# Kernel tuning notes

Measured on AMD Instinct MI355X. Metric: run time of the kernel, lower is better.

The kernel has to match this reference:

```python
import jax, jax.numpy as jnp
import numpy as np

B, C, H, W = 4, 128, 56, 56
K = 7
K2 = K * K
RATIO = 16


def _conv1x1(x, w, b=None):
    # x: [B,C,H,W], w: [O,C]
    y = jnp.einsum('oc,bchw->bohw', w, x)
    return y if b is None else y + b[None, :, None, None]


def _dwconv(x, w, dil, pad):
    # depthwise conv, w: [C,1,k,k]
    return jax.lax.conv_general_dilated(
        x, w, window_strides=(1, 1), padding=[(pad, pad), (pad, pad)],
        rhs_dilation=(dil, dil), feature_group_count=x.shape[1],
        dimension_numbers=('NCHW', 'OIHW', 'NCHW'))


def _bn(x, s, b):
    # inference-mode BatchNorm folded to per-channel affine
    return x * s[None, :, None, None] + b[None, :, None, None]


def setup_inputs() -> dict:
    key = jax.random.key(0)
    ks = jax.random.split(key, 16)
    w = 0.05  # weight scale
    inp = {
        'x_up': jax.random.normal(ks[0], (B, C, H, W), jnp.float32),
        'x_skip': jax.random.normal(ks[1], (B, C, H, W), jnp.float32),
        'wq': jax.random.normal(ks[2], (C, C), jnp.float32) * w,
        'bq': jnp.zeros((C,), jnp.float32),
        'wk': jax.random.normal(ks[3], (C, C), jnp.float32) * w,
        'bk': jnp.zeros((C,), jnp.float32),
        'wv': jax.random.normal(ks[4], (C, C), jnp.float32) * w,
        'bv': jnp.zeros((C,), jnp.float32),
        'ww': jax.random.normal(ks[5], (K2, 49), jnp.float32) * w,
        'bw': jnp.zeros((K2,), jnp.float32),
        'lk_w': jax.random.normal(ks[6], (C, 1, K, K), jnp.float32) * 0.1,
        'lk_bn_s': jax.random.uniform(ks[7], (C,), jnp.float32, 0.5, 1.5),
        'lk_bn_b': jnp.zeros((C,), jnp.float32),
        'dw5': jax.random.normal(ks[8], (C, 1, 5, 5), jnp.float32) * 0.1,
        'bn5_s': jax.random.uniform(ks[7], (C,), jnp.float32, 0.5, 1.5),
        'bn5_b': jnp.zeros((C,), jnp.float32),
        'dw3a': jax.random.normal(ks[9], (C, 1, 3, 3), jnp.float32) * 0.1,
        'bn3a_s': jax.random.uniform(ks[9], (C,), jnp.float32, 0.5, 1.5),
        'bn3a_b': jnp.zeros((C,), jnp.float32),
        'dw3b': jax.random.normal(ks[10], (C, 1, 3, 3), jnp.float32) * 0.1,
        'bn3b_s': jax.random.uniform(ks[10], (C,), jnp.float32, 0.5, 1.5),
        'bn3b_b': jnp.zeros((C,), jnp.float32),
        'dw3c': jax.random.normal(ks[11], (C, 1, 3, 3), jnp.float32) * 0.1,
        'bn3c_s': jax.random.uniform(ks[11], (C,), jnp.float32, 0.5, 1.5),
        'bn3c_b': jnp.zeros((C,), jnp.float32),
        'lepe_bn_s': jax.random.uniform(ks[12], (C,), jnp.float32, 0.5, 1.5),
        'lepe_bn_b': jnp.zeros((C,), jnp.float32),
        'gate_w': jax.random.normal(ks[13], (C, C), jnp.float32) * w,
        'gate_bn_s': jax.random.uniform(ks[13], (C,), jnp.float32, 0.5, 1.5),
        'gate_bn_b': jnp.zeros((C,), jnp.float32),
        'fus_w': jax.random.normal(ks[14], (C, C), jnp.float32) * w,
        'fus_b': jnp.zeros((C,), jnp.float32),
        'ca_w1': jax.random.normal(ks[15], (C // RATIO, C), jnp.float32) * w,
        'ca_w2': jax.random.normal(ks[15], (C, C // RATIO), jnp.float32) * w,
        'res_scale': jnp.ones((1,), jnp.float32),
    }
    return inp


def _forward(x_up, x_skip, wq, bq, wk, bk, wv, bv, ww, bw,
             lk_w, lk_bn_s, lk_bn_b, dw5, bn5_s, bn5_b,
             dw3a, bn3a_s, bn3a_b, dw3b, bn3b_s, bn3b_b, dw3c, bn3c_s, bn3c_b,
             lepe_bn_s, lepe_bn_b, gate_w, gate_bn_s, gate_bn_b,
             fus_w, fus_b, ca_w1, ca_w2, res_scale):
    identity = x_skip

    # ---- lepe: DilatedReparamBlock (lk 7x7 dw + 4 dilated dw branches, each BN) + final BN
    out = _bn(_dwconv(x_skip, lk_w, 1, 3), lk_bn_s, lk_bn_b)
    out = out + _bn(_dwconv(x_skip, dw5, 1, 2), bn5_s, bn5_b)    # k=5, d=1
    out = out + _bn(_dwconv(x_skip, dw3a, 1, 1), bn3a_s, bn3a_b)  # k=3, d=1
    out = out + _bn(_dwconv(x_skip, dw3b, 2, 2), bn3b_s, bn3b_b)  # k=3, d=2
    out = out + _bn(_dwconv(x_skip, dw3c, 3, 3), bn3c_s, bn3c_b)  # k=3, d=3
    lepe = _bn(out, lepe_bn_s, lepe_bn_b)

    # ---- gate: 1x1 conv (no bias) -> BN -> SiLU
    gate = jax.nn.silu(_bn(_conv1x1(x_skip, gate_w), gate_bn_s, gate_bn_b))

    # ---- q / k / v
    query = _conv1x1(x_skip, wq, bq)                              # [B,C,H,W]
    # AdaptiveAvgPool2d(7): H,W divisible by 7 -> block mean
    pooled = x_up.reshape(B, C, 7, H // 7, 7, W // 7).mean(axis=(3, 5))  # [B,C,7,7]
    key_t = _conv1x1(pooled, wk, bk).reshape(B, C, 49)            # [B,C,49]
    value = _conv1x1(x_skip, wv, bv)                              # [B,C,H,W]

    # ---- attention over 49 pooled key tokens
    scale = float(C) ** -0.5
    q_r = query.reshape(B, C, H * W).transpose(0, 2, 1)           # [B,HW,C]
    attn = jax.nn.softmax(jnp.einsum('bnc,bcl->bnl', q_r, key_t) * scale, axis=-1)
    attn_r = attn.transpose(0, 2, 1).reshape(B, 49, H, W)         # [B,49,H,W]
    dyn_w = jnp.einsum('ol,blhw->bohw', ww, attn_r) + bw[None, :, None, None]  # [B,K2,H,W]

    # ---- unfold value (k=7, pad=3), torch layout: channel-major, (kh,kw) row-major
    pad = K // 2
    vp = jnp.pad(value, ((0, 0), (0, 0), (pad, pad), (pad, pad)))
    patches = jnp.stack([vp[:, :, i:i + H, j:j + W]
                         for i in range(K) for j in range(K)], axis=2)  # [B,C,K2,H,W]
    mixed = jnp.einsum('bkhw,bckhw->bchw', dyn_w, patches)

    x_fused = _conv1x1(mixed, fus_w, fus_b) + lepe

    # ---- channel attention (shared MLP on avg & max pooled)
    avg = x_fused.mean(axis=(2, 3))                               # [B,C]
    mx = x_fused.max(axis=(2, 3))                                 # [B,C]
    def ca_mlp(v):
        return jnp.einsum('cr,br->bc', ca_w2, jax.nn.relu(jnp.einsum('rc,bc->br', ca_w1, v)))
    ca = jax.nn.sigmoid(ca_mlp(avg) + ca_mlp(mx))[:, :, None, None]
    x_fused = ca * x_fused

    return gate * x_fused + identity * res_scale


def reference(x_up, x_skip, wq, bq, wk, bk, wv, bv, ww, bw,
              lk_w, lk_bn_s, lk_bn_b, dw5, bn5_s, bn5_b,
              dw3a, bn3a_s, bn3a_b, dw3b, bn3b_s, bn3b_b, dw3c, bn3c_s, bn3c_b,
              lepe_bn_s, lepe_bn_b, gate_w, gate_bn_s, gate_bn_b,
              fus_w, fus_b, ca_w1, ca_w2, res_scale):
    return _forward(x_up, x_skip, wq, bq, wk, bk, wv, bv, ww, bw,
                    lk_w, lk_bn_s, lk_bn_b, dw5, bn5_s, bn5_b,
                    dw3a, bn3a_s, bn3a_b, dw3b, bn3b_s, bn3b_b, dw3c, bn3c_s, bn3c_b,
                    lepe_bn_s, lepe_bn_b, gate_w, gate_bn_s, gate_bn_b,
                    fus_w, fus_b, ca_w1, ca_w2, res_scale)
```

## Files before the change

### kernel.cpp

```cpp
#include <hip/hip_runtime.h>

typedef unsigned int u32;

#define HW 3136
#define SCALE 0.08838834764831843f

#define OFF_W7    0
#define OFF_BIAS  6272
#define OFF_POOL  6400
#define OFF_MT    31488
#define OFF_D     56576
#define OFF_AVG   56772
#define OFF_MAXU  57284
#define OFF_CA    57796
#define OFF_WC    58308
#define OFF_BC    74692
#define OFF_WQKT  74820
#define OFF_DQ    91204
#define OFF_VB    91332
#define OFF_S0    91460
#define OFF_FV    91464
#define OFF_DYN   1697096
#define OFF_XF    2311752

struct Params {
  const float *x_up, *x_skip, *wq, *bq, *wk, *bk, *wv, *bv, *ww, *bw;
  const float *lk_w, *lk_s, *lk_b, *dw5, *s5, *b5, *dw3a, *s3a, *b3a,
              *dw3b, *s3b, *b3b, *dw3c, *s3c, *b3c, *lepe_s, *lepe_b;
  const float *gate_w, *gate_s, *gate_b, *fus_w, *fus_b, *ca_w1, *ca_w2, *res;
  float* W;
  float* out;
};

__device__ __forceinline__ u32 fenc(float f){
  union{float f; u32 u;} v; v.f = f;
  return (v.u & 0x80000000u) ? ~v.u : (v.u | 0x80000000u);
}
__device__ __forceinline__ float fdec(u32 u){
  union{float f; u32 uu;} v;
  v.uu = (u & 0x80000000u) ? (u ^ 0x80000000u) : ~u;
  return v.f;
}

__global__ __launch_bounds__(256) void k_prep_w(Params P){
  float* W = P.W;
  const int tid = threadIdx.x, blk = blockIdx.x;
  if (blk < 64){
    const int o = blk*2 + (tid >> 7), c = tid & 127;
    float a = 0.f;
    #pragma unroll 8
    for (int m=0;m<128;++m) a += P.fus_w[o*128+m] * P.wv[m*128+c];
    W[OFF_WC + o*128 + c] = a;
  } else if (blk < 128){
    const int c = (blk-64)*2 + (tid >> 7), k = tid & 127;
    float a = 0.f;
    #pragma unroll 8
    for (int o=0;o<128;++o) a += P.wq[o*128+k] * P.wk[o*128+c];
    W[OFF_WQKT + c*128 + k] = a;
  } else if (blk == 128){
    for (int idx = tid; idx < 6272; idx += 256){
      const int c = idx/49, k = idx%49;
      const int dy = k/7 - 3, dx = k%7 - 3;
      float w = P.lk_s[c] * P.lk_w[c*49 + k];
      if (dy>=-2 && dy<=2 && dx>=-2 && dx<=2)
        w += P.s5[c] * P.dw5[c*25 + (dy+2)*5 + (dx+2)];
      if (dy>=-1 && dy<=1 && dx>=-1 && dx<=1)
        w += P.s3a[c] * P.dw3a[c*9 + (dy+1)*3 + (dx+1)];
      if ((dy==-2||dy==0||dy==2) && (dx==-2||dx==0||dx==2))
        w += P.s3b[c] * P.dw3b[c*9 + (dy/2+1)*3 + (dx/2+1)];
      if ((dy==-3||dy==0||dy==3) && (dx==-3||dx==0||dx==3))
        w += P.s3c[c] * P.dw3c[c*9 + (dy/3+1)*3 + (dx/3+1)];
      W[OFF_W7 + idx] = P.lepe_s[c] * w;
    }
    if (tid < 128){
      const float bs = P.lk_b[tid] + P.b5[tid] + P.b3a[tid] + P.b3b[tid] + P.b3c[tid];
      W[OFF_BIAS + tid] = P.lepe_s[tid] * bs + P.lepe_b[tid] + P.fus_b[tid];
    }
    for (int i = tid; i < 512; i += 256){
      W[OFF_AVG + i] = 0.f;
      ((u32*)W + OFF_MAXU)[i] = fenc(-1e30f);
    }
  } else {
    if (tid < 128){
      float bc = 0.f, dq = 0.f, vb = 0.f;
      #pragma unroll 8
      for (int m=0;m<128;++m){
        bc += P.fus_w[tid*128+m] * P.bv[m];
        dq += P.wq[m*128+tid] * P.bk[m];
        vb += P.bq[m] * P.wk[m*128+tid];
      }
      W[OFF_BC + tid] = bc;
      W[OFF_DQ + tid] = dq;
      W[OFF_VB + tid] = vb;
      if (tid == 0){
        float s = 0.f;
        for (int m=0;m<128;++m) s += P.bq[m]*P.bk[m];
        W[OFF_S0] = s;
      }
    }
  }
}

__global__ __launch_bounds__(256) void k_pool(Params P){
  __shared__ float pl[3136];
  __shared__ float part[208];
  float* W = P.W;
  const int tid = threadIdx.x, blk = blockIdx.x;
  const int b = blk >> 7, c = blk & 127;
  const float* src = P.x_up + (size_t)(b*128 + c)*HW;
  for (int idx = tid; idx < 784; idx += 256)
    *(float4*)&pl[idx*4] = *(const float4*)(src + idx*4);
  __syncthreads();
  if (tid < 196){
    const int l = tid >> 2, s = tid & 3;
    const int i = l/7, j = l%7;
    float sm = 0.f;
    #pragma unroll
    for (int r=0;r<2;++r){
      const int base = (8*i + 2*s + r)*56 + 8*j;
      #pragma unroll
      for (int e=0;e<8;++e) sm += pl[base+e];
    }
    part[tid] = sm;
  }
  __syncthreads();
  if (tid < 49){
    const float sm = part[tid*4] + part[tid*4+1] + part[tid*4+2] + part[tid*4+3];
    W[OFF_POOL + (size_t)(b*128+c)*49 + tid] = sm * (1.f/64.f);
  }
}

__global__ __launch_bounds__(128) void k_mt(Params P){
  __shared__ float pc[128], red[128];
  float* W = P.W;
  const int b = blockIdx.x / 49, l = blockIdx.x % 49;
  const int t = threadIdx.x;
  pc[t] = W[OFF_POOL + (size_t)(b*128+t)*49 + l];
  __syncthreads();
  float acc = W[OFF_DQ + t];
  #pragma unroll 8
  for (int c=0;c<128;++c) acc += W[OFF_WQKT + c*128 + t] * pc[c];
  W[OFF_MT + (size_t)b*6272 + t*49 + l] = acc * SCALE;
  red[t] = W[OFF_VB + t] * pc[t];
  __syncthreads();
  if (t < 64) red[t] += red[t+64];
  __syncthreads();
  if (t < 32) red[t] += red[t+32];
  __syncthreads();
  if (t < 16) red[t] += red[t+16];
  __syncthreads();
  if (t < 8) red[t] += red[t+8];
  __syncthreads();
  if (t < 4) red[t] += red[t+4];
  __syncthreads();
  if (t == 0)
    W[OFF_D + b*49 + l] = (red[0]+red[1]+red[2]+red[3] + W[OFF_S0]) * SCALE;
}

__global__ __launch_bounds__(256) void k_gemm(Params P){
  __shared__ float xl[128][20];
  __shared__ float wl[32][133];
  float* W = P.W;
  const int tid = threadIdx.x;
  const int x = blockIdx.x, xcd = x & 7;
  const int b = xcd >> 1;
  const int p0 = ((xcd & 1) + 2*(x >> 3)) * 16;
  const float* __restrict__ wsrc = W + OFF_WC;

  for (int idx = tid; idx < 512; idx += 256){
    const int c = idx >> 2, pq = idx & 3;
    *(float4*)&xl[c][pq*4] =
        *(const float4*)(P.x_skip + (size_t)(b*128+c)*HW + p0 + pq*4);
  }

  const int oq = tid >> 2, pq = tid & 3;
  const int o0 = oq*2, px = pq*4;
  const float i0 = W[OFF_BC + o0], i1 = W[OFF_BC + o0 + 1];
  float a0[4], a1[4];
  #pragma unroll
  for (int j=0;j<4;++j){ a0[j]=i0; a1[j]=i1; }

  for (int g=0; g<4; ++g){
    __syncthreads();
    for (int idx = tid; idx < 1024; idx += 256){
      const int o = idx >> 3, kq = idx & 7;
      const float4 v = *(const float4*)(wsrc + (size_t)o*128 + g*32 + kq*4);
      wl[kq*4+0][o] = v.x; wl[kq*4+1][o] = v.y;
      wl[kq*4+2][o] = v.z; wl[kq*4+3][o] = v.w;
    }
    __syncthreads();
    #pragma unroll 8
    for (int k=0;k<32;++k){
      const float2 w2 = *(const float2*)&wl[k][o0];
      const float4 x4 = *(const float4*)&xl[g*32+k][px];
      const float xv[4] = {x4.x,x4.y,x4.z,x4.w};
      #pragma unroll
      for (int j=0;j<4;++j){ a0[j] += w2.x*xv[j]; a1[j] += w2.y*xv[j]; }
    }
  }
  float4 v0 = {a0[0],a0[1],a0[2],a0[3]};
  float4 v1 = {a1[0],a1[1],a1[2],a1[3]};
  *(float4*)(W + OFF_FV + (size_t)(b*128+o0  )*HW + p0 + px) = v0;
  *(float4*)(W + OFF_FV + (size_t)(b*128+o0+1)*HW + p0 + px) = v1;
}

__global__ __launch_bounds__(256) void k_attn(Params P){
  __shared__ float xl[128][16];
  __shared__ float mtl[6272];
  __shared__ float wwl[2401];
  __shared__ float attl[16][52];
  __shared__ float dvl[52];
  float* W = P.W;
  const int tid = threadIdx.x;
  const int x = blockIdx.x, xcd = x & 7;
  const int b = xcd >> 1;
  const int p0 = ((xcd & 1) + 2*(x >> 3)) * 16;

  for (int idx = tid; idx < 512; idx += 256){
    const int c = idx >> 2, pq = idx & 3;
    *(float4*)&xl[c][pq*4] =
        *(const float4*)(P.x_skip + (size_t)(b*128+c)*HW + p0 + pq*4);
  }
  for (int idx = tid; idx < 1568; idx += 256)
    *(float4*)&mtl[idx*4] = *(const float4*)(W + OFF_MT + (size_t)b*6272 + idx*4);
  for (int idx = tid; idx < 600; idx += 256)
    *(float4*)&wwl[idx*4] = *(const float4*)(P.ww + idx*4);
  if (tid == 0) wwl[2400] = P.ww[2400];
  if (tid < 49) dvl[tid] = W[OFF_D + b*49 + tid];
  __syncthreads();

  const int px = tid >> 4, sub = tid & 15;
  const int l0 = sub, l1 = sub+16, l2 = sub+32, l3 = sub+48;
  const int l3c = (l3 < 49) ? l3 : 48;
  float lv0 = dvl[l0], lv1 = dvl[l1], lv2 = dvl[l2];
  float lv3 = (l3 < 49) ? dvl[l3] : -1e30f;
  float a3 = 0.f;
  #pragma unroll 4
  for (int c=0;c<128;++c){
    const float xv = xl[c][px];
    lv0 += mtl[c*49+l0]*xv;
    lv1 += mtl[c*49+l1]*xv;
    lv2 += mtl[c*49+l2]*xv;
    a3  += mtl[c*49+l3c]*xv;
  }
  if (l3 < 49) lv3 += a3;

  float m = fmaxf(fmaxf(lv0, lv1), fmaxf(lv2, lv3));
  #pragma unroll
  for (int d=1; d<16; d<<=1) m = fmaxf(m, __shfl_xor(m, d, 64));
  const float e0 = __expf(lv0-m), e1 = __expf(lv1-m), e2 = __expf(lv2-m);
  const float e3 = (l3 < 49) ? __expf(lv3-m) : 0.f;
  float s = e0+e1+e2+e3;
  #pragma unroll
  for (int d=1; d<16; d<<=1) s += __shfl_xor(s, d, 64);
  const float inv = 1.f / s;
  attl[px][l0] = e0*inv;
  attl[px][l1] = e1*inv;
  attl[px][l2] = e2*inv;
  if (l3 < 49) attl[px][l3] = e3*inv;
  __syncthreads();

  #pragma unroll
  for (int j=0;j<4;++j){
    const int oo = sub + 16*j;
    if (oo < 49){
      float a = P.bw[oo];
      #pragma unroll 7
      for (int l=0;l<49;++l) a += wwl[oo*49+l] * attl[px][l];
      W[OFF_DYN + (size_t)(b*49+oo)*HW + p0 + px] = a;
    }
  }
}

__global__ __launch_bounds__(256) void k_mix(Params P){
  __shared__ float fvs[2][20][64];
  __shared__ float xss[2][20][64];
  __shared__ float w7s[2][49];
  float* W = P.W;
  const int tid = threadIdx.x;
  const int blk = blockIdx.x, xcd = blk & 7;
  const int b = xcd >> 1;
  const int idx2 = blk >> 3;
  const int cp = idx2 >> 1;
  const int qt = (xcd & 1) + 2*(idx2 & 1);
  const int c0 = cp*2, r0 = qt*14;

  for (int idx = tid; idx < 1280; idx += 256){
    const int a2 = idx / 320;
    const int ch = a2 & 1, arr = a2 >> 1;
    const int rem = idx % 320;
    const int rr = rem >> 4, cq = rem & 15;
    const int gr = r0 - 3 + rr, gc0 = cq*4 - 4;
    float4 v = {0.f,0.f,0.f,0.f};
    if ((unsigned)gr < 56u){
      const float* src = arr ? (P.x_skip + (size_t)(b*128 + c0 + ch)*HW + gr*56)
                             : (W + OFF_FV + (size_t)(b*128 + c0 + ch)*HW + gr*56);
      if (gc0 >= 0 && gc0 + 3 < 56){
        v = *(const float4*)(src + gc0);
      } else {
        float t[4];
        #pragma unroll
        for (int e=0;e<4;++e){
          const int gc = gc0 + e;
          t[e] = ((unsigned)gc < 56u) ? src[gc] : 0.f;
        }
        v.x=t[0]; v.y=t[1]; v.z=t[2]; v.w=t[3];
      }
    }
    if (arr) *(float4*)&xss[ch][rr][cq*4] = v;
    else     *(float4*)&fvs[ch][rr][cq*4] = v;
  }
  if (tid < 98) w7s[tid/49][tid%49] = W[OFF_W7 + (c0 + tid/49)*49 + tid%49];
  __syncthreads();

  const bool act = tid < 196;
  const int row = tid / 14, q = tid % 14;
  const int q4 = q*4;
  const int grow = r0 + row;
  float acc[2][4];
  {
    const float b0 = W[OFF_BIAS + c0], b1 = W[OFF_BIAS + c0 + 1];
    #pragma unroll
    for (int e=0;e<4;++e){ acc[0][e] = b0; acc[1][e] = b1; }
  }
  if (act){
    const float* dynb = W + OFF_DYN + (size_t)b*49*HW + grow*56 + q4;
    #pragma unroll
    for (int i=0;i<7;++i){
      float4 dr[7];
      #pragma unroll
      for (int j=0;j<7;++j)
        dr[j] = *(const float4*)(dynb + (size_t)(i*7+j)*HW);
      #pragma unroll
      for (int ch=0;ch<2;++ch){
        float fw[12], xw[12];
        {
          float4 t;
          t = *(const float4*)&fvs[ch][row+i][q4];    fw[0]=t.x;fw[1]=t.y;fw[2]=t.z;fw[3]=t.w;
          t = *(const float4*)&fvs[ch][row+i][q4+4];  fw[4]=t.x;fw[5]=t.y;fw[6]=t.z;fw[7]=t.w;
          t = *(const float4*)&fvs[ch][row+i][q4+8];  fw[8]=t.x;fw[9]=t.y;fw[10]=t.z;fw[11]=t.w;
          t = *(const float4*)&xss[ch][row+i][q4];    xw[0]=t.x;xw[1]=t.y;xw[2]=t.z;xw[3]=t.w;
          t = *(const float4*)&xss[ch][row+i][q4+4];  xw[4]=t.x;xw[5]=t.y;xw[6]=t.z;xw[7]=t.w;
          t = *(const float4*)&xss[ch][row+i][q4+8];  xw[8]=t.x;xw[9]=t.y;xw[10]=t.z;xw[11]=t.w;
        }
        #pragma unroll
        for (int j=0;j<7;++j){
          const float4 dv = dr[j];
          const float wv = w7s[ch][i*7+j];
          acc[ch][0] += dv.x*fw[j+1] + wv*xw[j+1];
          acc[ch][1] += dv.y*fw[j+2] + wv*xw[j+2];
          acc[ch][2] += dv.z*fw[j+3] + wv*xw[j+3];
          acc[ch][3] += dv.w*fw[j+4] + wv*xw[j+4];
        }
      }
    }
    #pragma unroll
    for (int ch=0;ch<2;++ch){
      float4 v = {acc[ch][0], acc[ch][1], acc[ch][2], acc[ch][3]};
      *(float4*)(W + OFF_XF + (size_t)(b*128 + c0 + ch)*HW + grow*56 + q4) = v;
    }
  }
  #pragma unroll
  for (int ch=0;ch<2;++ch){
    float s = act ? (acc[ch][0]+acc[ch][1]+acc[ch][2]+acc[ch][3]) : 0.f;
    float mm = act ? fmaxf(fmaxf(acc[ch][0],acc[ch][1]),
                           fmaxf(acc[ch][2],acc[ch][3])) : -1e30f;
    #pragma unroll
    for (int d=1; d<64; d<<=1){
      s += __shfl_xor(s, d, 64);
      mm = fmaxf(mm, __shfl_xor(mm, d, 64));
    }
    if ((tid & 63) == 0){
      atomicAdd(W + OFF_AVG + b*128 + c0 + ch, s);
      atomicMax((u32*)W + OFF_MAXU + b*128 + c0 + ch, fenc(mm));
    }
  }
}

__global__ __launch_bounds__(512) void k_ca(Params P){
  __shared__ float avl[512], mxl[512], hl[64];
  float* W = P.W;
  const int tid = threadIdx.x;
  avl[tid] = W[OFF_AVG + tid] * (1.f/3136.f);
  mxl[tid] = fdec(((u32*)W + OFF_MAXU)[tid]);
  __syncthreads();
  if (tid < 64){
    const int b = tid >> 4, which = (tid >> 3) & 1, r = tid & 7;
    const float* v = (which ? mxl : avl) + b*128;
    float a = 0.f;
    const float4* wr = (const float4*)(P.ca_w1 + r*128);
    for (int k0=0;k0<32;++k0){
      const float4 w4 = wr[k0];
      a += w4.x*v[k0*4] + w4.y*v[k0*4+1] + w4.z*v[k0*4+2] + w4.w*v[k0*4+3];
    }
    hl[tid] = fmaxf(a, 0.f);
  }
  __syncthreads();
  {
    const int b = tid >> 7, c = tid & 127;
    float a = 0.f;
    #pragma unroll
    for (int r=0;r<8;++r) a += P.ca_w2[c*8+r] * (hl[b*16+r] + hl[b*16+8+r]);
    W[OFF_CA + tid] = 1.f/(1.f + __expf(-a));
  }
}

__global__ __launch_bounds__(256) void k_final(Params P){
  __shared__ float xl[128][20];
  __shared__ float wl[32][133];
  float* W = P.W;
  const int tid = threadIdx.x;
  const int x = blockIdx.x, xcd = x & 7;
  const int b = xcd >> 1;
  const int p0 = ((xcd & 1) + 2*(x >> 3)) * 16;

  for (int idx = tid; idx < 512; idx += 256){
    const int c = idx >> 2, pq = idx & 3;
    *(float4*)&xl[c][pq*4] =
        *(const float4*)(P.x_skip + (size_t)(b*128+c)*HW + p0 + pq*4);
  }

  const int oq = tid >> 2, pq = tid & 3;
  const int o0 = oq*2, px = pq*4;
  float a0[4] = {0.f,0.f,0.f,0.f}, a1[4] = {0.f,0.f,0.f,0.f};

  for (int g=0; g<4; ++g){
    __syncthreads();
    for (int idx = tid; idx < 1024; idx += 256){
      const int o = idx >> 3, kq = idx & 7;
      const float4 v = *(const float4*)(P.gate_w + (size_t)o*128 + g*32 + kq*4);
      wl[kq*4+0][o] = v.x; wl[kq*4+1][o] = v.y;
      wl[kq*4+2][o] = v.z; wl[kq*4+3][o] = v.w;
    }
    __syncthreads();
    #pragma unroll 8
    for (int k=0;k<32;++k){
      const float2 w2 = *(const float2*)&wl[k][o0];
      const float4 x4 = *(const float4*)&xl[g*32+k][px];
      const float xv[4] = {x4.x,x4.y,x4.z,x4.w};
      #pragma unroll
      for (int j=0;j<4;++j){ a0[j] += w2.x*xv[j]; a1[j] += w2.y*xv[j]; }
    }
  }
  const float s0 = P.gate_s[o0], s1 = P.gate_s[o0+1];
  const float c0 = P.gate_b[o0], c1 = P.gate_b[o0+1];
  const float ca0 = W[OFF_CA + b*128 + o0], ca1 = W[OFF_CA + b*128 + o0 + 1];
  const float res = P.res[0];
  const float4 xf0 = *(const float4*)(W + OFF_XF + (size_t)(b*128+o0  )*HW + p0 + px);
  const float4 xf1 = *(const float4*)(W + OFF_XF + (size_t)(b*128+o0+1)*HW + p0 + px);
  const float4 sk0 = *(const float4*)&xl[o0][px];
  const float4 sk1 = *(const float4*)&xl[o0+1][px];
  float g0[4] = {a0[0],a0[1],a0[2],a0[3]};
  float g1[4] = {a1[0],a1[1],a1[2],a1[3]};
  #pragma unroll
  for (int j=0;j<4;++j){
    float y0 = s0*g0[j] + c0, y1 = s1*g1[j] + c1;
    g0[j] = y0 / (1.f + __expf(-y0));
    g1[j] = y1 / (1.f + __expf(-y1));
  }
  float4 o0v, o1v;
  o0v.x = g0[0]*ca0*xf0.x + sk0.x*res;
  o0v.y = g0[1]*ca0*xf0.y + sk0.y*res;
  o0v.z = g0[2]*ca0*xf0.z + sk0.z*res;
  o0v.w = g0[3]*ca0*xf0.w + sk0.w*res;
  o1v.x = g1[0]*ca1*xf1.x + sk1.x*res;
  o1v.y = g1[1]*ca1*xf1.y + sk1.y*res;
  o1v.z = g1[2]*ca1*xf1.z + sk1.z*res;
  o1v.w = g1[3]*ca1*xf1.w + sk1.w*res;
  *(float4*)(P.out + (size_t)(b*128+o0  )*HW + p0 + px) = o0v;
  *(float4*)(P.out + (size_t)(b*128+o0+1)*HW + p0 + px) = o1v;
}

extern "C" void kernel_launch(void* const* d_in, const int* in_sizes, int n_in,
                              void* d_out, int out_size, void* d_ws, size_t ws_size,
                              hipStream_t stream){
  Params P;
  const float* const* in = (const float* const*)d_in;
  P.x_up = in[0];  P.x_skip = in[1]; P.wq = in[2];  P.bq = in[3];
  P.wk = in[4];    P.bk = in[5];     P.wv = in[6];  P.bv = in[7];
  P.ww = in[8];    P.bw = in[9];
  P.lk_w = in[10]; P.lk_s = in[11];  P.lk_b = in[12];
  P.dw5 = in[13];  P.s5 = in[14];    P.b5 = in[15];
  P.dw3a = in[16]; P.s3a = in[17];   P.b3a = in[18];
  P.dw3b = in[19]; P.s3b = in[20];   P.b3b = in[21];
  P.dw3c = in[22]; P.s3c = in[23];   P.b3c = in[24];
  P.lepe_s = in[25]; P.lepe_b = in[26];
  P.gate_w = in[27]; P.gate_s = in[28]; P.gate_b = in[29];
  P.fus_w = in[30];  P.fus_b = in[31];
  P.ca_w1 = in[32];  P.ca_w2 = in[33]; P.res = in[34];
  P.W = (float*)d_ws;
  P.out = (float*)d_out;

  hipLaunchKernelGGL(k_prep_w, dim3(130), dim3(256), 0, stream, P);
  hipLaunchKernelGGL(k_pool,   dim3(512), dim3(256), 0, stream, P);
  hipLaunchKernelGGL(k_mt,     dim3(196), dim3(128), 0, stream, P);
  hipLaunchKernelGGL(k_gemm,   dim3(784), dim3(256), 0, stream, P);
  hipLaunchKernelGGL(k_attn,   dim3(784), dim3(256), 0, stream, P);
  hipLaunchKernelGGL(k_mix,    dim3(1024),dim3(256), 0, stream, P);
  hipLaunchKernelGGL(k_ca,     dim3(1),   dim3(512), 0, stream, P);
  hipLaunchKernelGGL(k_final,  dim3(784), dim3(256), 0, stream, P);
}
```

Baseline: 272.2 us.

## Merge kernels: fold pooling into prep, gemm into attention, CA into final

Merges the pooling kernel into the weight-prep kernel as extra blocks, fuses the value 1x1 GEMM into the attention kernel (reusing one shared buffer for the weight tiles and then the MT matrix), and folds the tiny single-block channel-attention MLP into the final kernel, where each block recomputes it for its batch. This cuts the launch count from eight to five and removes the serial one-block k_ca stage. In exchange, every final block redoes the small MLP, and the fused attention kernel keeps the larger shared-memory footprint, which may limit occupancy.

```diff
diff --git a/kernel.cpp b/kernel.cpp
--- a/kernel.cpp
+++ b/kernel.cpp
@@ -12,7 +12,6 @@
 #define OFF_D     56576
 #define OFF_AVG   56772
 #define OFF_MAXU  57284
-#define OFF_CA    57796
 #define OFF_WC    58308
 #define OFF_BC    74692
 #define OFF_WQKT  74820
@@ -42,22 +41,47 @@
   return v.f;
 }
 
-__global__ __launch_bounds__(256) void k_prep_w(Params P){
+__global__ __launch_bounds__(256) void k_prep(Params P){
+  __shared__ float pl[3136];
+  __shared__ float part[208];
   float* W = P.W;
   const int tid = threadIdx.x, blk = blockIdx.x;
-  if (blk < 64){
-    const int o = blk*2 + (tid >> 7), c = tid & 127;
+  if (blk < 512){
+    const int b = blk >> 7, c = blk & 127;
+    const float* src = P.x_up + (size_t)(b*128 + c)*HW;
+    for (int idx = tid; idx < 784; idx += 256)
+      *(float4*)&pl[idx*4] = *(const float4*)(src + idx*4);
+    __syncthreads();
+    if (tid < 196){
+      const int l = tid >> 2, s = tid & 3;
+      const int i = l/7, j = l%7;
+      float sm = 0.f;
+      #pragma unroll
+      for (int r=0;r<2;++r){
+        const int base = (8*i + 2*s + r)*56 + 8*j;
+        #pragma unroll
+        for (int e=0;e<8;++e) sm += pl[base+e];
+      }
+      part[tid] = sm;
+    }
+    __syncthreads();
+    if (tid < 49){
+      const float sm = part[tid*4] + part[tid*4+1] + part[tid*4+2] + part[tid*4+3];
+      W[OFF_POOL + (size_t)(b*128+c)*49 + tid] = sm * (1.f/64.f);
+    }
+  } else if (blk < 576){
+    const int o = (blk-512)*2 + (tid >> 7), c = tid & 127;
     float a = 0.f;
     #pragma unroll 8
     for (int m=0;m<128;++m) a += P.fus_w[o*128+m] * P.wv[m*128+c];
     W[OFF_WC + o*128 + c] = a;
-  } else if (blk < 128){
-    const int c = (blk-64)*2 + (tid >> 7), k = tid & 127;
+  } else if (blk < 640){
+    const int c = (blk-576)*2 + (tid >> 7), k = tid & 127;
     float a = 0.f;
     #pragma unroll 8
     for (int o=0;o<128;++o) a += P.wq[o*128+k] * P.wk[o*128+c];
     W[OFF_WQKT + c*128 + k] = a;
-  } else if (blk == 128){
+  } else if (blk == 640){
     for (int idx = tid; idx < 6272; idx += 256){
       const int c = idx/49, k = idx%49;
       const int dy = k/7 - 3, dx = k%7 - 3;
@@ -101,35 +125,6 @@
   }
 }
 
-__global__ __launch_bounds__(256) void k_pool(Params P){
-  __shared__ float pl[3136];
-  __shared__ float part[208];
-  float* W = P.W;
-  const int tid = threadIdx.x, blk = blockIdx.x;
-  const int b = blk >> 7, c = blk & 127;
-  const float* src = P.x_up + (size_t)(b*128 + c)*HW;
-  for (int idx = tid; idx < 784; idx += 256)
-    *(float4*)&pl[idx*4] = *(const float4*)(src + idx*4);
-  __syncthreads();
-  if (tid < 196){
-    const int l = tid >> 2, s = tid & 3;
-    const int i = l/7, j = l%7;
-    float sm = 0.f;
-    #pragma unroll
-    for (int r=0;r<2;++r){
-      const int base = (8*i + 2*s + r)*56 + 8*j;
-      #pragma unroll
-      for (int e=0;e<8;++e) sm += pl[base+e];
-    }
-    part[tid] = sm;
-  }
-  __syncthreads();
-  if (tid < 49){
-    const float sm = part[tid*4] + part[tid*4+1] + part[tid*4+2] + part[tid*4+3];
-    W[OFF_POOL + (size_t)(b*128+c)*49 + tid] = sm * (1.f/64.f);
-  }
-}
-
 __global__ __launch_bounds__(128) void k_mt(Params P){
   __shared__ float pc[128], red[128];
   float* W = P.W;
@@ -157,56 +152,9 @@
     W[OFF_D + b*49 + l] = (red[0]+red[1]+red[2]+red[3] + W[OFF_S0]) * SCALE;
 }
 
-__global__ __launch_bounds__(256) void k_gemm(Params P){
+__global__ __launch_bounds__(256) void k_qvattn(Params P){
   __shared__ float xl[128][20];
-  __shared__ float wl[32][133];
-  float* W = P.W;
-  const int tid = threadIdx.x;
-  const int x = blockIdx.x, xcd = x & 7;
-  const int b = xcd >> 1;
-  const int p0 = ((xcd & 1) + 2*(x >> 3)) * 16;
-  const float* __restrict__ wsrc = W + OFF_WC;
-
-  for (int idx = tid; idx < 512; idx += 256){
-    const int c = idx >> 2, pq = idx & 3;
-    *(float4*)&xl[c][pq*4] =
-        *(const float4*)(P.x_skip + (size_t)(b*128+c)*HW + p0 + pq*4);
-  }
-
-  const int oq = tid >> 2, pq = tid & 3;
-  const int o0 = oq*2, px = pq*4;
-  const float i0 = W[OFF_BC + o0], i1 = W[OFF_BC + o0 + 1];
-  float a0[4], a1[4];
-  #pragma unroll
-  for (int j=0;j<4;++j){ a0[j]=i0; a1[j]=i1; }
-
-  for (int g=0; g<4; ++g){
-    __syncthreads();
-    for (int idx = tid; idx < 1024; idx += 256){
-      const int o = idx >> 3, kq = idx & 7;
-      const float4 v = *(const float4*)(wsrc + (size_t)o*128 + g*32 + kq*4);
-      wl[kq*4+0][o] = v.x; wl[kq*4+1][o] = v.y;
-      wl[kq*4+2][o] = v.z; wl[kq*4+3][o] = v.w;
-    }
-    __syncthreads();
-    #pragma unroll 8
-    for (int k=0;k<32;++k){
-      const float2 w2 = *(const float2*)&wl[k][o0];
-      const float4 x4 = *(const float4*)&xl[g*32+k][px];
-      const float xv[4] = {x4.x,x4.y,x4.z,x4.w};
-      #pragma unroll
-      for (int j=0;j<4;++j){ a0[j] += w2.x*xv[j]; a1[j] += w2.y*xv[j]; }
-    }
-  }
-  float4 v0 = {a0[0],a0[1],a0[2],a0[3]};
-  float4 v1 = {a1[0],a1[1],a1[2],a1[3]};
-  *(float4*)(W + OFF_FV + (size_t)(b*128+o0  )*HW + p0 + px) = v0;
-  *(float4*)(W + OFF_FV + (size_t)(b*128+o0+1)*HW + p0 + px) = v1;
-}
-
-__global__ __launch_bounds__(256) void k_attn(Params P){
-  __shared__ float xl[128][16];
-  __shared__ float mtl[6272];
+  __shared__ float sh[6272];
   __shared__ float wwl[2401];
   __shared__ float attl[16][52];
   __shared__ float dvl[52];
@@ -221,12 +169,45 @@
     *(float4*)&xl[c][pq*4] =
         *(const float4*)(P.x_skip + (size_t)(b*128+c)*HW + p0 + pq*4);
   }
-  for (int idx = tid; idx < 1568; idx += 256)
-    *(float4*)&mtl[idx*4] = *(const float4*)(W + OFF_MT + (size_t)b*6272 + idx*4);
   for (int idx = tid; idx < 600; idx += 256)
     *(float4*)&wwl[idx*4] = *(const float4*)(P.ww + idx*4);
   if (tid == 0) wwl[2400] = P.ww[2400];
   if (tid < 49) dvl[tid] = W[OFF_D + b*49 + tid];
+
+  const int oq = tid >> 2, pq = tid & 3;
+  const int o0 = oq*2, pxa = pq*4;
+  const float i0 = W[OFF_BC + o0], i1 = W[OFF_BC + o0 + 1];
+  float a0[4], a1[4];
+  #pragma unroll
+  for (int j=0;j<4;++j){ a0[j]=i0; a1[j]=i1; }
+  for (int g=0; g<4; ++g){
+    __syncthreads();
+    for (int idx = tid; idx < 1024; idx += 256){
+      const int o = idx >> 3, kq = idx & 7;
+      const float4 v = *(const float4*)(W + OFF_WC + (size_t)o*128 + g*32 + kq*4);
+      sh[(kq*4+0)*133+o] = v.x; sh[(kq*4+1)*133+o] = v.y;
+      sh[(kq*4+2)*133+o] = v.z; sh[(kq*4+3)*133+o] = v.w;
+    }
+    __syncthreads();
+    #pragma unroll 8
+    for (int k=0;k<32;++k){
+      const float2 w2 = *(const float2*)&sh[k*133+o0];
+      const float4 x4 = *(const float4*)&xl[g*32+k][pxa];
+      const float xv[4] = {x4.x,x4.y,x4.z,x4.w};
+      #pragma unroll
+      for (int j=0;j<4;++j){ a0[j] += w2.x*xv[j]; a1[j] += w2.y*xv[j]; }
+    }
+  }
+  {
+    float4 v0 = {a0[0],a0[1],a0[2],a0[3]};
+    float4 v1 = {a1[0],a1[1],a1[2],a1[3]};
+    *(float4*)(W + OFF_FV + (size_t)(b*128+o0  )*HW + p0 + pxa) = v0;
+    *(float4*)(W + OFF_FV + (size_t)(b*128+o0+1)*HW + p0 + pxa) = v1;
+  }
+
+  __syncthreads();
+  for (int idx = tid; idx < 1568; idx += 256)
+    *(float4*)&sh[idx*4] = *(const float4*)(W + OFF_MT + (size_t)b*6272 + idx*4);
   __syncthreads();
 
   const int px = tid >> 4, sub = tid & 15;
@@ -238,10 +219,10 @@
   #pragma unroll 4
   for (int c=0;c<128;++c){
     const float xv = xl[c][px];
-    lv0 += mtl[c*49+l0]*xv;
-    lv1 += mtl[c*49+l1]*xv;
-    lv2 += mtl[c*49+l2]*xv;
-    a3  += mtl[c*49+l3c]*xv;
+    lv0 += sh[c*49+l0]*xv;
+    lv1 += sh[c*49+l1]*xv;
+    lv2 += sh[c*49+l2]*xv;
+    a3  += sh[c*49+l3c]*xv;
   }
   if (l3 < 49) lv3 += a3;
 
@@ -377,37 +358,10 @@
   }
 }
 
-__global__ __launch_bounds__(512) void k_ca(Params P){
-  __shared__ float avl[512], mxl[512], hl[64];
-  float* W = P.W;
-  const int tid = threadIdx.x;
-  avl[tid] = W[OFF_AVG + tid] * (1.f/3136.f);
-  mxl[tid] = fdec(((u32*)W + OFF_MAXU)[tid]);
-  __syncthreads();
-  if (tid < 64){
-    const int b = tid >> 4, which = (tid >> 3) & 1, r = tid & 7;
-    const float* v = (which ? mxl : avl) + b*128;
-    float a = 0.f;
-    const float4* wr = (const float4*)(P.ca_w1 + r*128);
-    for (int k0=0;k0<32;++k0){
-      const float4 w4 = wr[k0];
-      a += w4.x*v[k0*4] + w4.y*v[k0*4+1] + w4.z*v[k0*4+2] + w4.w*v[k0*4+3];
-    }
-    hl[tid] = fmaxf(a, 0.f);
-  }
-  __syncthreads();
-  {
-    const int b = tid >> 7, c = tid & 127;
-    float a = 0.f;
-    #pragma unroll
-    for (int r=0;r<8;++r) a += P.ca_w2[c*8+r] * (hl[b*16+r] + hl[b*16+8+r]);
-    W[OFF_CA + tid] = 1.f/(1.f + __expf(-a));
-  }
-}
-
 __global__ __launch_bounds__(256) void k_final(Params P){
   __shared__ float xl[128][20];
   __shared__ float wl[32][133];
+  __shared__ float hl[16], cal[128];
   float* W = P.W;
   const int tid = threadIdx.x;
   const int x = blockIdx.x, xcd = x & 7;
@@ -418,6 +372,24 @@
     const int c = idx >> 2, pq = idx & 3;
     *(float4*)&xl[c][pq*4] =
         *(const float4*)(P.x_skip + (size_t)(b*128+c)*HW + p0 + pq*4);
+  }
+  if (tid < 16){
+    const int r = tid & 7, which = tid >> 3;
+    float a = 0.f;
+    #pragma unroll 8
+    for (int c=0;c<128;++c){
+      const float v = which ? fdec(((u32*)W + OFF_MAXU)[b*128+c])
+                            : W[OFF_AVG + b*128+c] * (1.f/3136.f);
+      a += P.ca_w1[r*128+c] * v;
+    }
+    hl[tid] = fmaxf(a, 0.f);
+  }
+  __syncthreads();
+  if (tid < 128){
+    float a = 0.f;
+    #pragma unroll
+    for (int r=0;r<8;++r) a += P.ca_w2[tid*8+r] * (hl[r] + hl[8+r]);
+    cal[tid] = 1.f/(1.f + __expf(-a));
   }
 
   const int oq = tid >> 2, pq = tid & 3;
@@ -444,7 +416,7 @@
   }
   const float s0 = P.gate_s[o0], s1 = P.gate_s[o0+1];
   const float c0 = P.gate_b[o0], c1 = P.gate_b[o0+1];
-  const float ca0 = W[OFF_CA + b*128 + o0], ca1 = W[OFF_CA + b*128 + o0 + 1];
+  const float ca0 = cal[o0], ca1 = cal[o0+1];
   const float res = P.res[0];
   const float4 xf0 = *(const float4*)(W + OFF_XF + (size_t)(b*128+o0  )*HW + p0 + px);
   const float4 xf1 = *(const float4*)(W + OFF_XF + (size_t)(b*128+o0+1)*HW + p0 + px);
@@ -491,12 +463,9 @@
   P.W = (float*)d_ws;
   P.out = (float*)d_out;
 
-  hipLaunchKernelGGL(k_prep_w, dim3(130), dim3(256), 0, stream, P);
-  hipLaunchKernelGGL(k_pool,   dim3(512), dim3(256), 0, stream, P);
+  hipLaunchKernelGGL(k_prep,   dim3(642), dim3(256), 0, stream, P);
   hipLaunchKernelGGL(k_mt,     dim3(196), dim3(128), 0, stream, P);
-  hipLaunchKernelGGL(k_gemm,   dim3(784), dim3(256), 0, stream, P);
-  hipLaunchKernelGGL(k_attn,   dim3(784), dim3(256), 0, stream, P);
+  hipLaunchKernelGGL(k_qvattn, dim3(784), dim3(256), 0, stream, P);
   hipLaunchKernelGGL(k_mix,    dim3(1024),dim3(256), 0, stream, P);
-  hipLaunchKernelGGL(k_ca,     dim3(1),   dim3(512), 0, stream, P);
   hipLaunchKernelGGL(k_final,  dim3(784), dim3(256), 0, stream, P);
 }
```

After: 280.5 us. 3.0% more time.
